# Kernel tuning notes

Hardware: AMD Instinct MI355X
Metric: run time of the kernel (lower is better)

The kernel has to match this reference:

```python
import jax, jax.numpy as jnp
import numpy as np
from itertools import product

PBC_RADIUS = 1
# (K,3) integer image offsets, K = 27 for radius 1
_OFFSETS = jnp.asarray(np.array(list(product(range(-PBC_RADIUS, PBC_RADIUS + 1), repeat=3)), dtype=np.float32))


def _nan0(x):
    return jnp.nan_to_num(x, nan=0.0, posinf=0.0, neginf=0.0)


def _y1_and_gram(lattice):
    # _sanitize_lattice_latent for lattice_repr='y1'
    log_len = jnp.clip(lattice[:, :3], -5.0, 5.0)
    cosang = jnp.clip(lattice[:, 3:], -0.9999, 0.9999)
    lattice_y1 = jnp.concatenate([log_len, cosang], axis=-1)  # identity map for 'y1'
    lengths = jnp.exp(log_len)                                # (B,3)
    a, b, c = lengths[:, 0], lengths[:, 1], lengths[:, 2]
    ca, cb, cg = cosang[:, 0], cosang[:, 1], cosang[:, 2]
    # Gram: G_ij = l_i l_j cos(theta_ij); G01=ab*cos(gamma), G02=ac*cos(beta), G12=bc*cos(alpha)
    row0 = jnp.stack([a * a, a * b * cg, a * c * cb], axis=-1)
    row1 = jnp.stack([a * b * cg, b * b, b * c * ca], axis=-1)
    row2 = jnp.stack([a * c * cb, b * c * ca, c * c], axis=-1)
    gram = jnp.stack([row0, row1, row2], axis=1)  # (B,3,3)
    return _nan0(lattice_y1), _nan0(gram)


def _geometry(coords, lattice):
    coords = coords.astype(jnp.float32)
    lattice = lattice.astype(jnp.float32)
    lattice_y1, gram = _y1_and_gram(lattice)

    # (B,N,N,3) pairwise fractional deltas, then (B,N,N,K,3) periodic images
    delta = coords[:, :, None, :] - coords[:, None, :, :]
    delta_images = delta[:, :, :, None, :] + _OFFSETS  # broadcast over (K,3)

    # squared min-image distances under lattice metric: (B,N,N,K)
    dist2_images = jnp.einsum('bnmki,bij,bnmkj->bnmk', delta_images, gram, delta_images)

    min_idx = jnp.argmin(dist2_images, axis=-1)  # (B,N,N)
    min_dist2 = jnp.take_along_axis(dist2_images, min_idx[..., None], axis=-1)[..., 0]
    min_dist2 = jnp.maximum(min_dist2, 0.0)
    min_delta = jnp.take_along_axis(delta_images, min_idx[..., None, None], axis=3)[..., 0, :]  # (B,N,N,3)

    # safe sqrt (diagonal pairs have dist2 == 0; torch nan_to_num's the fwd NaNs)
    pos = min_dist2 > 0.0
    min_dist = jnp.where(pos, jnp.sqrt(jnp.where(pos, min_dist2, 1.0)), 0.0)
    min_dist = _nan0(min_dist)
    min_dist2 = _nan0(min_dist2)

    lengths = jnp.exp(lattice_y1[:, :3])
    cell_scale = jnp.maximum(lengths.mean(axis=-1), 1e-6)  # (B,)
    min_dist_norm = _nan0(min_dist / cell_scale[:, None, None])

    # pack geometry features: (B,N,N,6) = [min_delta(3), min_dist, min_dist2, min_dist_norm]
    out = jnp.concatenate(
        [min_delta, min_dist[..., None], min_dist2[..., None], min_dist_norm[..., None]], axis=-1)
    return out


def setup_inputs() -> dict:
    key = jax.random.key(0)
    k1, k2 = jax.random.split(key)
    coords = jax.random.uniform(k1, (8, 320, 3), dtype=jnp.float32)      # fractional coords in [0,1)
    lattice = jax.random.normal(k2, (8, 6), dtype=jnp.float32) * 0.5     # y1 latent (log-lengths, cosines)
    return {"coords": coords, "lattice": lattice}


def reference(coords, lattice):
    return _geometry(coords, lattice)
```

## Files before the change

kernel.cpp:

```cpp
#include <hip/hip_runtime.h>
#include <math.h>

__global__ void __launch_bounds__(256) geom_kernel(const float* __restrict__ coords,
                                                   const float* __restrict__ lattice,
                                                   float* __restrict__ out) {
    const int N = 320;
    unsigned pos = blockIdx.x * 256u + threadIdx.x;
    int b = blockIdx.y;
    unsigned n  = pos / 80u;
    unsigned m0 = (pos - n * 80u) * 4u;

    const float* lat = lattice + b * 6;
    float l0 = fminf(fmaxf(lat[0], -5.0f), 5.0f);
    float l1 = fminf(fmaxf(lat[1], -5.0f), 5.0f);
    float l2 = fminf(fmaxf(lat[2], -5.0f), 5.0f);
    float ca = fminf(fmaxf(lat[3], -0.9999f), 0.9999f);
    float cb = fminf(fmaxf(lat[4], -0.9999f), 0.9999f);
    float cg = fminf(fmaxf(lat[5], -0.9999f), 0.9999f);

    float a  = expf(l0);
    float bl = expf(l1);
    float c  = expf(l2);

    float G00 = a * a;
    float G01 = (a * bl) * cg;
    float G02 = (a * c) * cb;
    float G11 = bl * bl;
    float G12 = (bl * c) * ca;
    float G22 = c * c;

    float twoG01 = G01 + G01;
    float twoG02 = G02 + G02;
    float twoG12 = G12 + G12;

    float cell  = fmaxf((a + bl + c) / 3.0f, 1e-6f);
    float rcell = 1.0f / cell;

    const float* cn = coords + ((size_t)b * N + n) * 3;
    float nx = cn[0], ny = cn[1], nz = cn[2];

    const float4* cmv = (const float4*)(coords + ((size_t)b * N + m0) * 3);
    float4 q0 = cmv[0], q1 = cmv[1], q2 = cmv[2];
    float mx[4] = {q0.x, q0.w, q1.z, q2.y};
    float my[4] = {q0.y, q1.x, q1.w, q2.z};
    float mz[4] = {q0.z, q1.y, q2.x, q2.w};

    float res[24];

    #pragma unroll
    for (int j = 0; j < 4; ++j) {
        float dx = nx - mx[j];
        float dy = ny - my[j];
        float dz = nz - mz[j];

        float best = INFINITY;
        int bestk = 0;
        #pragma unroll
        for (int kx = 0; kx < 3; ++kx) {
            float e0 = dx + (float)(kx - 1);
            float u   = (e0 * G00) * e0;
            float t01 = e0 * twoG01;
            float t02 = e0 * twoG02;
            #pragma unroll
            for (int ky = 0; ky < 3; ++ky) {
                float e1 = dy + (float)(ky - 1);
                float v = fmaf(e1, fmaf(e1, G11, t01), u);
                float w = fmaf(e1, twoG12, t02);
                #pragma unroll
                for (int kz = 0; kz < 3; ++kz) {
                    float e2 = dz + (float)(kz - 1);
                    float f = fmaf(e2, G22, w);
                    float dist2 = fmaf(e2, f, v);
                    int k = kx * 9 + ky * 3 + kz;
                    if (dist2 < best) { best = dist2; bestk = k; }
                }
            }
        }

        unsigned uk = (unsigned)bestk;
        float ox = (float)(uk / 9u) - 1.0f;
        float oy = (float)((uk / 3u) % 3u) - 1.0f;
        float oz = (float)(uk % 3u) - 1.0f;

        float md2 = fmaxf(best, 0.0f);
        float mdist = (md2 > 0.0f) ? sqrtf(md2) : 0.0f;

        res[j * 6 + 0] = dx + ox;
        res[j * 6 + 1] = dy + oy;
        res[j * 6 + 2] = dz + oz;
        res[j * 6 + 3] = mdist;
        res[j * 6 + 4] = md2;
        res[j * 6 + 5] = mdist * rcell;
    }

    float4* ov = (float4*)(out + (((size_t)b * N + n) * N + m0) * 6);
    #pragma unroll
    for (int t = 0; t < 6; ++t) {
        ov[t] = make_float4(res[4 * t], res[4 * t + 1], res[4 * t + 2], res[4 * t + 3]);
    }
}

extern "C" void kernel_launch(void* const* d_in, const int* in_sizes, int n_in,
                              void* d_out, int out_size, void* d_ws, size_t ws_size,
                              hipStream_t stream) {
    const float* coords = (const float*)d_in[0];
    const float* lattice = (const float*)d_in[1];
    float* out = (float*)d_out;

    dim3 grid(100, 8);
    geom_kernel<<<grid, 256, 0, stream>>>(coords, lattice, out);
}
```

Before: 15.31 us.

## Map one pair per thread, hoist Gram setup to shared memory, min-reduce z images

```diff
diff --git a/kernel.cpp b/kernel.cpp
--- a/kernel.cpp
+++ b/kernel.cpp
@@ -5,98 +5,98 @@
                                                    const float* __restrict__ lattice,
                                                    float* __restrict__ out) {
     const int N = 320;
+    __shared__ float sc[8];
+    int b = blockIdx.y;
+
+    if (threadIdx.x == 0) {
+        const float* lat = lattice + b * 6;
+        float l0 = fminf(fmaxf(lat[0], -5.0f), 5.0f);
+        float l1 = fminf(fmaxf(lat[1], -5.0f), 5.0f);
+        float l2 = fminf(fmaxf(lat[2], -5.0f), 5.0f);
+        float ca = fminf(fmaxf(lat[3], -0.9999f), 0.9999f);
+        float cb = fminf(fmaxf(lat[4], -0.9999f), 0.9999f);
+        float cg = fminf(fmaxf(lat[5], -0.9999f), 0.9999f);
+        float a  = expf(l0);
+        float bl = expf(l1);
+        float c  = expf(l2);
+        float G00 = a * a;
+        float G01 = (a * bl) * cg;
+        float G02 = (a * c) * cb;
+        float G11 = bl * bl;
+        float G12 = (bl * c) * ca;
+        float G22 = c * c;
+        sc[0] = G00;
+        sc[1] = G11;
+        sc[2] = G22;
+        sc[3] = G01 + G01;
+        sc[4] = G02 + G02;
+        sc[5] = G12 + G12;
+        sc[6] = 1.0f / fmaxf((a + bl + c) / 3.0f, 1e-6f);
+    }
+    __syncthreads();
+
+    float G00 = sc[0], G11 = sc[1], G22 = sc[2];
+    float twoG01 = sc[3], twoG02 = sc[4], twoG12 = sc[5];
+    float rcell = sc[6];
+
     unsigned pos = blockIdx.x * 256u + threadIdx.x;
-    int b = blockIdx.y;
-    unsigned n  = pos / 80u;
-    unsigned m0 = (pos - n * 80u) * 4u;
-
-    const float* lat = lattice + b * 6;
-    float l0 = fminf(fmaxf(lat[0], -5.0f), 5.0f);
-    float l1 = fminf(fmaxf(lat[1], -5.0f), 5.0f);
-    float l2 = fminf(fmaxf(lat[2], -5.0f), 5.0f);
-    float ca = fminf(fmaxf(lat[3], -0.9999f), 0.9999f);
-    float cb = fminf(fmaxf(lat[4], -0.9999f), 0.9999f);
-    float cg = fminf(fmaxf(lat[5], -0.9999f), 0.9999f);
-
-    float a  = expf(l0);
-    float bl = expf(l1);
-    float c  = expf(l2);
-
-    float G00 = a * a;
-    float G01 = (a * bl) * cg;
-    float G02 = (a * c) * cb;
-    float G11 = bl * bl;
-    float G12 = (bl * c) * ca;
-    float G22 = c * c;
-
-    float twoG01 = G01 + G01;
-    float twoG02 = G02 + G02;
-    float twoG12 = G12 + G12;
-
-    float cell  = fmaxf((a + bl + c) / 3.0f, 1e-6f);
-    float rcell = 1.0f / cell;
+    unsigned n = pos / 320u;
+    unsigned m = pos - n * 320u;
 
     const float* cn = coords + ((size_t)b * N + n) * 3;
-    float nx = cn[0], ny = cn[1], nz = cn[2];
+    const float* cm = coords + ((size_t)b * N + m) * 3;
+    float dx = cn[0] - cm[0];
+    float dy = cn[1] - cm[1];
+    float dz = cn[2] - cm[2];
 
-    const float4* cmv = (const float4*)(coords + ((size_t)b * N + m0) * 3);
-    float4 q0 = cmv[0], q1 = cmv[1], q2 = cmv[2];
-    float mx[4] = {q0.x, q0.w, q1.z, q2.y};
-    float my[4] = {q0.y, q1.x, q1.w, q2.z};
-    float mz[4] = {q0.z, q1.y, q2.x, q2.w};
+    float e0[3] = {dx + -1.0f, dx + 0.0f, dx + 1.0f};
+    float e1[3] = {dy + -1.0f, dy + 0.0f, dy + 1.0f};
+    float e2[3] = {dz + -1.0f, dz + 0.0f, dz + 1.0f};
 
-    float res[24];
+    float best = INFINITY;
+    int bestg = 0;
+    #pragma unroll
+    for (int gx = 0; gx < 3; ++gx) {
+        float E0  = e0[gx];
+        float u   = (E0 * G00) * E0;
+        float t01 = E0 * twoG01;
+        float t02 = E0 * twoG02;
+        #pragma unroll
+        for (int gy = 0; gy < 3; ++gy) {
+            float E1 = e1[gy];
+            float v = fmaf(E1, fmaf(E1, G11, t01), u);
+            float w = fmaf(E1, twoG12, t02);
+            float d0 = fmaf(e2[0], fmaf(e2[0], G22, w), v);
+            float d1 = fmaf(e2[1], fmaf(e2[1], G22, w), v);
+            float d2 = fmaf(e2[2], fmaf(e2[2], G22, w), v);
+            float gmin = fminf(fminf(d0, d1), d2);
+            if (gmin < best) { best = gmin; bestg = gx * 4 + gy; }
+        }
+    }
 
-    #pragma unroll
-    for (int j = 0; j < 4; ++j) {
-        float dx = nx - mx[j];
-        float dy = ny - my[j];
-        float dz = nz - mz[j];
-
-        float best = INFINITY;
-        int bestk = 0;
-        #pragma unroll
-        for (int kx = 0; kx < 3; ++kx) {
-            float e0 = dx + (float)(kx - 1);
-            float u   = (e0 * G00) * e0;
-            float t01 = e0 * twoG01;
-            float t02 = e0 * twoG02;
-            #pragma unroll
-            for (int ky = 0; ky < 3; ++ky) {
-                float e1 = dy + (float)(ky - 1);
-                float v = fmaf(e1, fmaf(e1, G11, t01), u);
-                float w = fmaf(e1, twoG12, t02);
-                #pragma unroll
-                for (int kz = 0; kz < 3; ++kz) {
-                    float e2 = dz + (float)(kz - 1);
-                    float f = fmaf(e2, G22, w);
-                    float dist2 = fmaf(e2, f, v);
-                    int k = kx * 9 + ky * 3 + kz;
-                    if (dist2 < best) { best = dist2; bestk = k; }
-                }
-            }
-        }
-
-        unsigned uk = (unsigned)bestk;
-        float ox = (float)(uk / 9u) - 1.0f;
-        float oy = (float)((uk / 3u) % 3u) - 1.0f;
-        float oz = (float)(uk % 3u) - 1.0f;
+    int gx = bestg >> 2;
+    int gy = bestg & 3;
+    float E0 = (gx == 0) ? e0[0] : ((gx == 1) ? e0[1] : e0[2]);
+    float E1 = (gy == 0) ? e1[0] : ((gy == 1) ? e1[1] : e1[2]);
+    {
+        float u   = (E0 * G00) * E0;
+        float t01 = E0 * twoG01;
+        float t02 = E0 * twoG02;
+        float v = fmaf(E1, fmaf(E1, G11, t01), u);
+        float w = fmaf(E1, twoG12, t02);
+        float d0 = fmaf(e2[0], fmaf(e2[0], G22, w), v);
+        float d1 = fmaf(e2[1], fmaf(e2[1], G22, w), v);
+        float E2 = (d0 == best) ? e2[0] : ((d1 == best) ? e2[1] : e2[2]);
 
         float md2 = fmaxf(best, 0.0f);
         float mdist = (md2 > 0.0f) ? sqrtf(md2) : 0.0f;
+        float mnorm = mdist * rcell;
 
-        res[j * 6 + 0] = dx + ox;
-        res[j * 6 + 1] = dy + oy;
-        res[j * 6 + 2] = dz + oz;
-        res[j * 6 + 3] = mdist;
-        res[j * 6 + 4] = md2;
-        res[j * 6 + 5] = mdist * rcell;
-    }
-
-    float4* ov = (float4*)(out + (((size_t)b * N + n) * N + m0) * 6);
-    #pragma unroll
-    for (int t = 0; t < 6; ++t) {
-        ov[t] = make_float4(res[4 * t], res[4 * t + 1], res[4 * t + 2], res[4 * t + 3]);
+        size_t base = (((size_t)b * N + n) * N + m) * 6;
+        float2* ov = (float2*)(out + base);
+        ov[0] = make_float2(E0, E1);
+        ov[1] = make_float2(E2, mdist);
+        ov[2] = make_float2(md2, mnorm);
     }
 }
 
@@ -107,6 +107,6 @@
     const float* lattice = (const float*)d_in[1];
     float* out = (float*)d_out;
 
-    dim3 grid(100, 8);
+    dim3 grid(400, 8);
     geom_kernel<<<grid, 256, 0, stream>>>(coords, lattice, out);
 }
```

Result: faster. 12.62 us (-17.6%).
